# Performance work log

Measured on AMD Instinct MI355X. Metric: run time of the kernel, lower is better.

Reference implementation:

```python
import jax, jax.numpy as jnp
import numpy as np

# Lorentz (hyperboloid) manifold, curvature parameter K: x0 = sqrt(K + ||x_space||^2)
K = 1.0
LN_EPS = 1e-5
PROJ_EPS = 1e-6
L, D, H, B, S, V = 12, 512, 8, 2, 1024, 50257
DH = D // H  # 64 space dims per head


def add_time(space):
    # lift space components onto the hyperboloid
    t = jnp.sqrt(jnp.sum(space * space, axis=-1, keepdims=True) + K)
    return jnp.concatenate([t, space], axis=-1)


def l_project(z):
    # renormalize an ambient vector onto the hyperboloid (Lorentz midpoint / LResNet normalization)
    inner = -jnp.square(z[..., :1]) + jnp.sum(jnp.square(z[..., 1:]), axis=-1, keepdims=True)
    return jnp.sqrt(K) * z / jnp.sqrt(jnp.clip(-inner, PROJ_EPS, None))


def l_layernorm(x, g, b):
    # LayerNorm on the space part, recompute time
    s = x[..., 1:]
    mu = jnp.mean(s, axis=-1, keepdims=True)
    var = jnp.var(s, axis=-1, keepdims=True)
    s = (s - mu) * jax.lax.rsqrt(var + LN_EPS) * g + b
    return add_time(s)


def setup_inputs() -> dict:
    key = jax.random.key(0)
    ks = jax.random.split(key, 12)
    std_in = D ** -0.5
    std_out = (2 * D * L) ** -0.5  # out_proj_std from the torch init
    inp = {}
    inp['text_tokens'] = jax.random.randint(ks[0], (B, S), 0, V)
    inp['embed_table'] = jax.random.normal(ks[1], (V, D - 1), jnp.float32) * 0.02
    inp['Wq'] = jax.random.normal(ks[2], (L, D, D), jnp.float32) * std_in
    inp['bq'] = jnp.zeros((L, D), jnp.float32)
    inp['Wk'] = jax.random.normal(ks[3], (L, D, D), jnp.float32) * std_in
    inp['bk'] = jnp.zeros((L, D), jnp.float32)
    inp['Wv'] = jax.random.normal(ks[4], (L, D, D), jnp.float32) * std_in
    inp['bv'] = jnp.zeros((L, D), jnp.float32)
    inp['Wo'] = jax.random.normal(ks[5], (L, H * (DH + 1), D - 1), jnp.float32) * std_in
    inp['bo'] = jnp.zeros((L, D - 1), jnp.float32)
    inp['ln1_g'] = jnp.ones((L, D - 1), jnp.float32)
    inp['ln1_b'] = jnp.zeros((L, D - 1), jnp.float32)
    inp['ln2_g'] = jnp.ones((L, D - 1), jnp.float32)
    inp['ln2_b'] = jnp.zeros((L, D - 1), jnp.float32)
    inp['Wfc'] = jax.random.normal(ks[6], (L, D, 4 * D - 1), jnp.float32) * std_in
    inp['bfc'] = jnp.zeros((L, 4 * D - 1), jnp.float32)
    inp['Wpr'] = jax.random.normal(ks[7], (L, 4 * D, D - 1), jnp.float32) * std_out
    inp['bpr'] = jnp.zeros((L, D - 1), jnp.float32)
    inp['res_w1'] = jnp.ones((L,), jnp.float32)
    inp['res_w2'] = jnp.ones((L,), jnp.float32)
    inp['Wfin'] = jax.random.normal(ks[8], (D, D - 1), jnp.float32) * std_in
    inp['bfin'] = jnp.zeros((D - 1,), jnp.float32)
    inp['lnf_g'] = jnp.ones((D - 1,), jnp.float32)
    inp['lnf_b'] = jnp.zeros((D - 1,), jnp.float32)
    return inp


def reference(text_tokens, embed_table, Wq, bq, Wk, bk, Wv, bv, Wo, bo, ln1_g, ln1_b,
              ln2_g, ln2_b, Wfc, bfc, Wpr, bpr, res_w1, res_w2, Wfin, bfin, lnf_g, lnf_b):
    b, s = text_tokens.shape
    scale = 1.0 / np.sqrt(DH)
    # LorentzEmbeddings: space-part lookup, time recomputed
    x = add_time(embed_table[text_tokens])  # [B, S, D]
    causal = jnp.tril(jnp.ones((s, s), bool))  # True = attend
    for i in range(L):
        # --- Lorentz multi-head self-attention ---
        lx = l_layernorm(x, ln1_g[i], ln1_b[i])
        q = add_time((lx @ Wq[i] + bq[i]).reshape(b, s, H, DH))  # [B,S,H,DH+1]
        k = add_time((lx @ Wk[i] + bk[i]).reshape(b, s, H, DH))
        v = add_time((lx @ Wv[i] + bv[i]).reshape(b, s, H, DH))
        qm = jnp.concatenate([-q[..., :1], q[..., 1:]], axis=-1)  # apply Minkowski metric
        linner = jnp.einsum('bihd,bjhd->bhij', qm, k)  # Lorentz inner product <q_i, k_j>_L
        scores = (2.0 * K + 2.0 * linner) * scale     # = -d_L^2(q,k)/sqrt(dh)
        scores = jnp.where(causal[None, None], scores, -1e9)
        a = jax.nn.softmax(scores, axis=-1)
        agg = jnp.einsum('bhij,bjhd->bihd', a, v)      # Lorentz centroid numerator
        agg = l_project(agg)                           # normalize back to hyperboloid
        ax = add_time(agg.reshape(b, s, H * (DH + 1)) @ Wo[i] + bo[i])  # heads-concat proj
        x = l_project(x + res_w1[i] * ax)              # LResNet residual 1
        # --- Lorentz MLP ---
        h = l_layernorm(x, ln2_g[i], ln2_b[i])
        h = add_time(h @ Wfc[i] + bfc[i])              # c_fc: D -> 4D ambient
        h = add_time(jax.nn.gelu(h[..., 1:]))          # LorentzActivation (GELU on space)
        h = add_time(h @ Wpr[i] + bpr[i])              # c_proj: 4D -> D ambient
        x = l_project(x + res_w2[i] * h)               # LResNet residual 2
    x = add_time(x @ Wfin + bfin)                      # final_proj
    x = l_layernorm(x, lnf_g, lnf_b)                   # ln_final
    return x
```

## Files before the change

kernel.cpp:

```cpp
#include <hip/hip_runtime.h>
#include <cstdint>

#define DEV __device__ __forceinline__

typedef _Float16 f16;
typedef _Float16 f16x8 __attribute__((ext_vector_type(8)));
typedef float f32x4 __attribute__((ext_vector_type(4)));
typedef unsigned int u32;

DEV void gll16(const void* g, void* l) {
  __builtin_amdgcn_global_load_lds((const __attribute__((address_space(1))) u32*)g,
                                   (__attribute__((address_space(3))) u32*)l, 16, 0, 0);
}

DEV float block_sum(float v, float* red) {
#pragma unroll
  for (int o = 32; o; o >>= 1) v += __shfl_xor(v, o);
  int w = threadIdx.x >> 6;
  __syncthreads();
  if ((threadIdx.x & 63) == 0) red[w] = v;
  __syncthreads();
  return red[0] + red[1] + red[2] + red[3];
}

__global__ void k_trans(const float* __restrict__ W0, f16* __restrict__ BT0, int K, int N, int Kpad,
                        size_t srcStride, size_t dstStride) {
  __shared__ float t[32][33];
  const float* W = W0 + (size_t)blockIdx.z * srcStride;
  f16* BT = BT0 + (size_t)blockIdx.z * dstStride;
  int n0 = blockIdx.x * 32, k0 = blockIdx.y * 32, tx = threadIdx.x, ty = threadIdx.y;
  for (int i = ty; i < 32; i += 8) {
    int k = k0 + i, n = n0 + tx;
    t[i][tx] = (k < K && n < N) ? W[(size_t)k * N + n] : 0.f;
  }
  __syncthreads();
  for (int i = ty; i < 32; i += 8)
    BT[(size_t)(n0 + i) * Kpad + k0 + tx] = (f16)t[tx][i];
}

__global__ void k_trans3(const float* __restrict__ Wq, const float* __restrict__ Wk,
                         const float* __restrict__ Wv, f16* __restrict__ BT) {
  __shared__ float t[32][33];
  const int layer = blockIdx.z / 3, typ = blockIdx.z % 3;
  const float* W = ((typ == 0) ? Wq : (typ == 1) ? Wk : Wv) + (size_t)layer * 262144;
  f16* dst = BT + (size_t)layer * 786432 + (size_t)typ * 262144;
  int n0 = blockIdx.x * 32, k0 = blockIdx.y * 32, tx = threadIdx.x, ty = threadIdx.y;
  for (int i = ty; i < 32; i += 8) t[i][tx] = W[(size_t)(k0 + i) * 512 + n0 + tx];
  __syncthreads();
  for (int i = ty; i < 32; i += 8) dst[(size_t)(n0 + i) * 512 + k0 + tx] = (f16)t[tx][i];
}

template <int BM, int BN, int EPI>
__launch_bounds__(256)
__global__ void k_gemm(const f16* __restrict__ A, const f16* __restrict__ BT,
                       int lda, int ldb, int klen,
                       float* __restrict__ O1, float* __restrict__ O2, int ldc,
                       const float* __restrict__ c0, const float* __restrict__ c1,
                       const float* __restrict__ c2, float* __restrict__ ssq,
                       f16* __restrict__ H1, f16* __restrict__ H2, f16* __restrict__ H3) {
  constexpr int FM = BM / 32, FN = BN / 32;
  __shared__ f16 sA[BM * 64];
  __shared__ f16 sB[BN * 64];
  const int tid = threadIdx.x, wid = tid >> 6, lane = tid & 63;
  const int l15 = lane & 15, l4 = lane >> 4;
  const int m0 = blockIdx.x * BM, n0 = blockIdx.y * BN;
  const int wm = wid >> 1, wn = wid & 1;
  const int kbeg = blockIdx.z * klen;
  f32x4 acc[FM][FN];
#pragma unroll
  for (int i = 0; i < FM; i++)
#pragma unroll
    for (int j = 0; j < FN; j++) acc[i][j] = (f32x4){0.f, 0.f, 0.f, 0.f};
  const size_t ldab = (size_t)lda * 2, ldbb = (size_t)ldb * 2;
  const int swz = ((lane & 7) ^ (lane >> 3)) * 16;
  const char* Ab = (const char*)A + (size_t)m0 * ldab + (size_t)(lane >> 3) * ldab + swz;
  const char* Bb = (const char*)BT + (size_t)n0 * ldbb + (size_t)(lane >> 3) * ldbb + swz;
  for (int k0 = kbeg; k0 < kbeg + klen; k0 += 64) {
    for (int i = wid; i < BM / 8; i += 4)
      gll16(Ab + (size_t)(i * 8) * ldab + (size_t)k0 * 2, (char*)sA + i * 1024);
    for (int i = wid; i < BN / 8; i += 4)
      gll16(Bb + (size_t)(i * 8) * ldbb + (size_t)k0 * 2, (char*)sB + i * 1024);
    __syncthreads();
#pragma unroll
    for (int kk = 0; kk < 2; kk++) {
      f16x8 af[FM], bf[FN];
#pragma unroll
      for (int i = 0; i < FM; i++) {
        int row = wm * (BM / 2) + i * 16 + l15;
        af[i] = *(const f16x8*)(sA + row * 64 + (((kk * 4 + l4) ^ (l15 & 7)) * 8));
      }
#pragma unroll
      for (int j = 0; j < FN; j++) {
        int row = wn * (BN / 2) + j * 16 + l15;
        bf[j] = *(const f16x8*)(sB + row * 64 + (((kk * 4 + l4) ^ (l15 & 7)) * 8));
      }
#pragma unroll
      for (int i = 0; i < FM; i++)
#pragma unroll
        for (int j = 0; j < FN; j++)
          acc[i][j] = __builtin_amdgcn_mfma_f32_16x16x32_f16(af[i], bf[j], acc[i][j], 0, 0, 0);
    }
    __syncthreads();
  }
  if (EPI == 0) {
#pragma unroll
    for (int i = 0; i < FM; i++) {
      int row0 = m0 + wm * (BM / 2) + i * 16 + l4 * 4;
#pragma unroll
      for (int j = 0; j < FN; j++) {
        int col = n0 + wn * (BN / 2) + j * 16 + l15;
#pragma unroll
        for (int r = 0; r < 4; r++) O1[(size_t)(row0 + r) * ldc + col] = acc[i][j][r];
      }
    }
  } else if (EPI == 1) {
    const int cb = (n0 >> 6) + wn;
    const int typ = cb >> 3, h = cb & 7;
    const float* bb = (typ == 0) ? c0 : (typ == 1) ? c1 : c2;
    float bias_j[FN];
#pragma unroll
    for (int j = 0; j < FN; j++) bias_j[j] = bb[h * 64 + j * 16 + l15];
    const float qs = (typ == 0) ? 0.25f : 1.0f;
#pragma unroll
    for (int i = 0; i < FM; i++) {
#pragma unroll
      for (int r = 0; r < 4; r++) {
        float y[FN];
        float ss = 0.f;
#pragma unroll
        for (int j = 0; j < FN; j++) {
          y[j] = acc[i][j][r] + bias_j[j];
          ss += y[j] * y[j];
        }
        ss += __shfl_xor(ss, 1); ss += __shfl_xor(ss, 2);
        ss += __shfl_xor(ss, 4); ss += __shfl_xor(ss, 8);
        float t = sqrtf(ss + 1.f);
        int row = m0 + wm * 64 + i * 16 + l4 * 4 + r;
        int b = row >> 10, s = row & 1023, bh = b * 8 + h;
        if (typ < 2) {
          f16* dst = (typ == 0) ? H1 : H2;
          size_t base = ((size_t)bh * 1024 + s) * 88;
#pragma unroll
          for (int j = 0; j < FN; j++) dst[base + j * 16 + l15] = (f16)(qs * y[j]);
          if (l15 == 0) dst[base + 64] = (f16)(qs * t);
        } else {
#pragma unroll
          for (int j = 0; j < FN; j++)
            H3[((size_t)bh * 80 + j * 16 + l15) * 1024 + s] = (f16)y[j];
          if (l15 == 0) H3[((size_t)bh * 80 + 64) * 1024 + s] = (f16)t;
        }
      }
    }
  } else if (EPI == 2) {
#pragma unroll
    for (int i = 0; i < FM; i++) {
#pragma unroll
      for (int r = 0; r < 4; r++) {
        int row = m0 + wm * 64 + i * 16 + l4 * 4 + r;
        float ss = 0.f;
#pragma unroll
        for (int j = 0; j < FN; j++) {
          int col = n0 + wn * 64 + j * 16 + l15;
          float gg = 0.f;
          if (col < 2047) {
            float yv = acc[i][j][r] + c0[col];
            float cc = yv * yv * yv;
            gg = 0.5f * yv * (1.f + tanhf(0.7978845608f * (yv + 0.044715f * cc)));
          }
          ss += gg * gg;
          H1[(size_t)row * 2048 + col] = (f16)gg;
        }
        ss += __shfl_xor(ss, 1); ss += __shfl_xor(ss, 2);
        ss += __shfl_xor(ss, 4); ss += __shfl_xor(ss, 8);
        if (l15 == 0) atomicAdd(ssq + row, ss);
      }
    }
  } else {
    float* O = blockIdx.z ? O2 : O1;
#pragma unroll
    for (int i = 0; i < FM; i++) {
#pragma unroll
      for (int r = 0; r < 4; r++) {
        int row = m0 + wm * (BM / 2) + i * 16 + l4 * 4 + r;
        float t = 0.f;
        if (blockIdx.z == 0) t = sqrtf(ssq[row] + 1.f);
#pragma unroll
        for (int j = 0; j < FN; j++) {
          int col = n0 + wn * (BN / 2) + j * 16 + l15;
          float v = acc[i][j][r];
          if (blockIdx.z == 0) v += t * ((col < 511) ? c0[col] : 0.f);
          O[(size_t)row * ldc + col] = v;
        }
      }
    }
  }
}

__global__ void k_embed(const int* __restrict__ tok, const float* __restrict__ tbl,
                        const float* __restrict__ g, const float* __restrict__ bsh,
                        float* __restrict__ x, f16* __restrict__ act) {
  __shared__ float red[4];
  const int m = blockIdx.x, tid = threadIdx.x;
  const float* e = tbl + (size_t)tok[m] * 511;
  float e0 = (tid < 511) ? e[tid] : 0.f;
  float e1 = (tid + 256 < 511) ? e[tid + 256] : 0.f;
  float s1 = block_sum(e0 + e1, red);
  float s2 = block_sum(e0 * e0 + e1 * e1, red);
  float t = sqrtf(s2 + 1.f);
  float* xr = x + (size_t)m * 512;
  if (tid == 0) xr[0] = t;
  if (tid < 511) xr[1 + tid] = e0;
  if (tid + 256 < 511) xr[257 + tid] = e1;
  float mu = s1 / 511.f;
  float var = s2 / 511.f - mu * mu;
  float inv = rsqrtf(var + 1e-5f);
  float n0 = (tid < 511) ? (e0 - mu) * inv * g[tid] + bsh[tid] : 0.f;
  float n1 = (tid + 256 < 511) ? (e1 - mu) * inv * g[tid + 256] + bsh[tid + 256] : 0.f;
  float sn = block_sum(n0 * n0 + n1 * n1, red);
  float t2 = sqrtf(sn + 1.f);
  f16* ar = act + (size_t)m * 512;
  if (tid == 0) ar[0] = (f16)t2;
  if (tid < 511) ar[1 + tid] = (f16)n0;
  if (tid + 256 < 511) ar[257 + tid] = (f16)n1;
}

__launch_bounds__(64)
__global__ void k_attn(const f16* __restrict__ qhat, const f16* __restrict__ khat,
                       const f16* __restrict__ vT, f16* __restrict__ ao) {
  __shared__ f16 sP[16 * 88];
  const int bid = blockIdx.x, bh = bid & 15, rt = 63 - (bid >> 4);
  const int lane = threadIdx.x, l15 = lane & 15, l4 = lane >> 4;
  const f16* qp = qhat + ((size_t)bh * 1024 + rt * 16) * 88;
  const f16* kp = khat + (size_t)bh * 1024 * 88;
  const f16* vp = vT + (size_t)bh * 80 * 1024;
  f16x8 qf0 = *(const f16x8*)(qp + l15 * 88 + l4 * 8);
  f16x8 qf1 = *(const f16x8*)(qp + l15 * 88 + 32 + l4 * 8);
  float qth[4];
#pragma unroll
  for (int r = 0; r < 4; r++) qth[r] = (float)qp[(l4 * 4 + r) * 88 + 64];
  f32x4 acc[5];
#pragma unroll
  for (int i = 0; i < 5; i++) acc[i] = (f32x4){0, 0, 0, 0};
  float mrun[4] = {-3e38f, -3e38f, -3e38f, -3e38f}, lrun[4] = {0, 0, 0, 0};
  const int nt = (rt >> 2) + 1;
  for (int jt = 0; jt < nt; ++jt) {
    const int j0 = jt * 64;
    const bool dt = (jt == nt - 1);
    f32x4 sc[4];
#pragma unroll
    for (int fn = 0; fn < 4; fn++) {
      const f16* kb = kp + (size_t)(j0 + fn * 16 + l15) * 88;
      f16x8 k0v = *(const f16x8*)(kb + l4 * 8);
      f16x8 k1v = *(const f16x8*)(kb + 32 + l4 * 8);
      f32x4 a = (f32x4){0, 0, 0, 0};
      a = __builtin_amdgcn_mfma_f32_16x16x32_f16(qf0, k0v, a, 0, 0, 0);
      a = __builtin_amdgcn_mfma_f32_16x16x32_f16(qf1, k1v, a, 0, 0, 0);
      sc[fn] = a;
    }
    float s[4][4];
#pragma unroll
    for (int fn = 0; fn < 4; fn++) {
      float ktc = (float)kp[(size_t)(j0 + fn * 16 + l15) * 88 + 64];
      int col = j0 + fn * 16 + l15;
#pragma unroll
      for (int r = 0; r < 4; r++) {
        int row = rt * 16 + l4 * 4 + r;
        float v = sc[fn][r] - qth[r] * ktc;
        s[fn][r] = (!dt || col <= row) ? v : -3e38f;
      }
    }
    float mnew[4], al[4], rs[4];
#pragma unroll
    for (int r = 0; r < 4; r++) {
      float t = fmaxf(fmaxf(s[0][r], s[1][r]), fmaxf(s[2][r], s[3][r]));
#pragma unroll
      for (int o = 8; o; o >>= 1) t = fmaxf(t, __shfl_xor(t, o));
      mnew[r] = fmaxf(mrun[r], t);
      al[r] = exp2f((mrun[r] - mnew[r]) * 1.44269504f);
      mrun[r] = mnew[r];
      rs[r] = 0.f;
    }
#pragma unroll
    for (int fn = 0; fn < 4; fn++)
#pragma unroll
      for (int r = 0; r < 4; r++) {
        float p = exp2f((s[fn][r] - mnew[r]) * 1.44269504f);
        rs[r] += p;
        sP[(l4 * 4 + r) * 88 + fn * 16 + l15] = (f16)p;
      }
#pragma unroll
    for (int r = 0; r < 4; r++) {
#pragma unroll
      for (int o = 8; o; o >>= 1) rs[r] += __shfl_xor(rs[r], o);
      lrun[r] = lrun[r] * al[r] + rs[r];
    }
#pragma unroll
    for (int fd = 0; fd < 5; fd++)
#pragma unroll
      for (int r = 0; r < 4; r++) acc[fd][r] *= al[r];
    __syncthreads();
#pragma unroll
    for (int ks = 0; ks < 2; ks++) {
      f16x8 pf = *(const f16x8*)(sP + l15 * 88 + ks * 32 + l4 * 8);
#pragma unroll
      for (int fd = 0; fd < 5; fd++) {
        f16x8 vf = *(const f16x8*)(vp + (size_t)(fd * 16 + l15) * 1024 + j0 + ks * 32 + l4 * 8);
        acc[fd] = __builtin_amdgcn_mfma_f32_16x16x32_f16(pf, vf, acc[fd], 0, 0, 0);
      }
    }
    __syncthreads();
  }
  const int b = bh >> 3, h = bh & 7;
#pragma unroll
  for (int r = 0; r < 4; r++) {
    float invl = 1.0f / lrun[r];
    float ss = 0.f;
    float ov[4];
#pragma unroll
    for (int fd = 0; fd < 4; fd++) {
      ov[fd] = acc[fd][r] * invl;
      ss += ov[fd] * ov[fd];
    }
#pragma unroll
    for (int o = 8; o; o >>= 1) ss += __shfl_xor(ss, o);
    float tv = acc[4][r] * invl;
    tv = __shfl(tv, lane & 48);
    float scp = rsqrtf(fmaxf(tv * tv - ss, 1e-6f));
    int row = rt * 16 + l4 * 4 + r;
    size_t rowbase = ((size_t)b * 1024 + row) * 576;
    size_t rb = rowbase + h * 65;
    if (l15 == 0) ao[rb] = (f16)(tv * scp);
#pragma unroll
    for (int fd = 0; fd < 4; fd++) ao[rb + 1 + fd * 16 + l15] = (f16)(ov[fd] * scp);
    for (int c = l15; c < 56; c += 16) ao[rowbase + 520 + c] = (f16)0.f;
  }
}

__global__ void k_resproj(float* __restrict__ x, const float* __restrict__ r1,
                          const float* __restrict__ r2, int useR2,
                          const float* __restrict__ bias, const float* __restrict__ resw, int li,
                          const float* __restrict__ g, const float* __restrict__ bsh,
                          f16* __restrict__ act, int applyLN, float* __restrict__ ssq) {
  __shared__ float red[4];
  const int m = blockIdx.x, tid = threadIdx.x;
  const float* ra = r1 + (size_t)m * 512;
  const float* rb = r2 + (size_t)m * 512;
  float* xr = x + (size_t)m * 512;
  const float rw = resw[li];
  if (tid == 0) ssq[m] = 0.f;
  float y0 = 0.f, y1 = 0.f;
  if (tid < 511) { y0 = ra[tid] + bias[tid]; if (useR2) y0 += rb[tid]; }
  if (tid + 256 < 511) { y1 = ra[tid + 256] + bias[tid + 256]; if (useR2) y1 += rb[tid + 256]; }
  float s2 = block_sum(y0 * y0 + y1 * y1, red);
  float tax = sqrtf(s2 + 1.f);
  float xt = xr[0];
  float u0 = (tid < 511) ? xr[1 + tid] + rw * y0 : 0.f;
  float u1 = (tid + 256 < 511) ? xr[257 + tid] + rw * y1 : 0.f;
  float ut = xt + rw * tax;
  float su = block_sum(u0 + u1, red);
  float su2 = block_sum(u0 * u0 + u1 * u1, red);
  float scp = rsqrtf(fmaxf(ut * ut - su2, 1e-6f));
  float nx0 = u0 * scp, nx1 = u1 * scp, nxt = ut * scp;
  if (tid == 0) xr[0] = nxt;
  if (tid < 511) xr[1 + tid] = nx0;
  if (tid + 256 < 511) xr[257 + tid] = nx1;
  f16* ar = act + (size_t)m * 512;
  if (applyLN) {
    float mu = su * scp / 511.f;
    float var = su2 * scp * scp / 511.f - mu * mu;
    float inv = rsqrtf(var + 1e-5f);
    float n0 = (tid < 511) ? (nx0 - mu) * inv * g[tid] + bsh[tid] : 0.f;
    float n1 = (tid + 256 < 511) ? (nx1 - mu) * inv * g[tid + 256] + bsh[tid + 256] : 0.f;
    float sn = block_sum(n0 * n0 + n1 * n1, red);
    float t2 = sqrtf(sn + 1.f);
    if (tid == 0) ar[0] = (f16)t2;
    if (tid < 511) ar[1 + tid] = (f16)n0;
    if (tid + 256 < 511) ar[257 + tid] = (f16)n1;
  } else {
    if (tid == 0) ar[0] = (f16)nxt;
    if (tid < 511) ar[1 + tid] = (f16)nx0;
    if (tid + 256 < 511) ar[257 + tid] = (f16)nx1;
  }
}

__global__ void k_final(const float* __restrict__ raw, const float* __restrict__ bias,
                        const float* __restrict__ g, const float* __restrict__ bsh,
                        float* __restrict__ out) {
  __shared__ float red[4];
  const int m = blockIdx.x, tid = threadIdx.x;
  const float* rr = raw + (size_t)m * 512;
  float y0 = (tid < 511) ? rr[tid] + bias[tid] : 0.f;
  float y1 = (tid + 256 < 511) ? rr[tid + 256] + bias[tid + 256] : 0.f;
  float s1 = block_sum(y0 + y1, red);
  float s2 = block_sum(y0 * y0 + y1 * y1, red);
  float mu = s1 / 511.f;
  float var = s2 / 511.f - mu * mu;
  float inv = rsqrtf(var + 1e-5f);
  float n0 = (tid < 511) ? (y0 - mu) * inv * g[tid] + bsh[tid] : 0.f;
  float n1 = (tid + 256 < 511) ? (y1 - mu) * inv * g[tid + 256] + bsh[tid + 256] : 0.f;
  float sn = block_sum(n0 * n0 + n1 * n1, red);
  float t2 = sqrtf(sn + 1.f);
  float* orow = out + (size_t)m * 512;
  if (tid == 0) orow[0] = t2;
  if (tid < 511) orow[1 + tid] = n0;
  if (tid + 256 < 511) orow[257 + tid] = n1;
}

extern "C" void kernel_launch(void* const* d_in, const int* in_sizes, int n_in,
                              void* d_out, int out_size, void* d_ws, size_t ws_size,
                              hipStream_t stream) {
  (void)in_sizes; (void)n_in; (void)out_size; (void)ws_size;
  const int* tok = (const int*)d_in[0];
  const float* etab = (const float*)d_in[1];
  const float* Wq = (const float*)d_in[2];
  const float* bq = (const float*)d_in[3];
  const float* Wk = (const float*)d_in[4];
  const float* bk = (const float*)d_in[5];
  const float* Wv = (const float*)d_in[6];
  const float* bv = (const float*)d_in[7];
  const float* Wo = (const float*)d_in[8];
  const float* bo = (const float*)d_in[9];
  const float* ln1g = (const float*)d_in[10];
  const float* ln1b = (const float*)d_in[11];
  const float* ln2g = (const float*)d_in[12];
  const float* ln2b = (const float*)d_in[13];
  const float* Wfc = (const float*)d_in[14];
  const float* bfc = (const float*)d_in[15];
  const float* Wpr = (const float*)d_in[16];
  const float* bpr = (const float*)d_in[17];
  const float* rw1 = (const float*)d_in[18];
  const float* rw2 = (const float*)d_in[19];
  const float* Wfin = (const float*)d_in[20];
  const float* bfin = (const float*)d_in[21];
  const float* lnfg = (const float*)d_in[22];
  const float* lnfb = (const float*)d_in[23];

  char* wsb = (char*)d_ws;
  size_t off = 0;
  auto alloc = [&](size_t bytes) -> char* {
    char* p = wsb + off;
    off = (off + bytes + 1023) & ~(size_t)1023;
    return p;
  };
  float* x = (float*)alloc(2048ull * 512 * 4);
  f16* actA = (f16*)alloc(2048ull * 512 * 2);
  float* raw1 = (float*)alloc(2048ull * 512 * 4);
  float* raw2 = (float*)alloc(2048ull * 512 * 4);
  float* ssq = (float*)alloc(2048ull * 4);
  f16* qhat = (f16*)alloc(16ull * 1024 * 88 * 2);
  f16* khat = (f16*)alloc(16ull * 1024 * 88 * 2);
  f16* vT = (f16*)alloc(16ull * 80 * 1024 * 2);
  f16* ao = (f16*)alloc(2048ull * 576 * 2);
  f16* fcact = (f16*)alloc(2048ull * 2048 * 2);
  f16* wqkvT = (f16*)alloc(12ull * 1536 * 512 * 2);
  f16* woT = (f16*)alloc(12ull * 512 * 576 * 2);
  f16* wfcT = (f16*)alloc(12ull * 2048 * 512 * 2);
  f16* wprT = (f16*)alloc(12ull * 512 * 2048 * 2);
  f16* wfinT = (f16*)alloc(512ull * 512 * 2);

  k_trans3<<<dim3(16, 16, 36), dim3(32, 8), 0, stream>>>(Wq, Wk, Wv, wqkvT);
  k_trans<<<dim3(16, 18, 12), dim3(32, 8), 0, stream>>>(Wo, woT, 520, 511, 576,
                                                        520ull * 511, 512ull * 576);
  k_trans<<<dim3(64, 16, 12), dim3(32, 8), 0, stream>>>(Wfc, wfcT, 512, 2047, 512,
                                                        512ull * 2047, 2048ull * 512);
  k_trans<<<dim3(16, 64, 12), dim3(32, 8), 0, stream>>>(Wpr + 511, wprT, 2047, 511, 2048,
                                                        2048ull * 511, 512ull * 2048);
  k_trans<<<dim3(16, 16, 1), dim3(32, 8), 0, stream>>>(Wfin, wfinT, 512, 511, 512, 0, 0);

  k_embed<<<2048, 256, 0, stream>>>(tok, etab, ln1g, ln1b, x, actA);

  for (int li = 0; li < 12; li++) {
    const f16* wqkvT_l = wqkvT + (size_t)li * 1536 * 512;
    const f16* woT_l = woT + (size_t)li * 512 * 576;
    const f16* wfcT_l = wfcT + (size_t)li * 2048 * 512;
    const f16* wprT_l = wprT + (size_t)li * 512 * 2048;
    const float* Wpr_l = Wpr + (size_t)li * 2048 * 511;
    const float* bq_l = bq + (size_t)li * 512;
    const float* bk_l = bk + (size_t)li * 512;
    const float* bv_l = bv + (size_t)li * 512;
    const float* bo_l = bo + (size_t)li * 511;
    const float* bfc_l = bfc + (size_t)li * 2047;
    const float* bpr_l = bpr + (size_t)li * 511;
    const float* ln2g_l = ln2g + (size_t)li * 511;
    const float* ln2b_l = ln2b + (size_t)li * 511;

    k_gemm<128, 128, 1><<<dim3(16, 12, 1), 256, 0, stream>>>(
        actA, wqkvT_l, 512, 512, 512, nullptr, nullptr, 0,
        bq_l, bk_l, bv_l, nullptr, qhat, khat, vT);
    k_attn<<<1024, 64, 0, stream>>>(qhat, khat, vT, ao);
    k_gemm<64, 64, 0><<<dim3(32, 8, 1), 256, 0, stream>>>(
        ao, woT_l, 576, 576, 576, raw1, nullptr, 512,
        nullptr, nullptr, nullptr, nullptr, nullptr, nullptr, nullptr);
    k_resproj<<<2048, 256, 0, stream>>>(x, raw1, raw1, 0, bo_l, rw1, li,
                                        ln2g_l, ln2b_l, actA, 1, ssq);
    k_gemm<128, 128, 2><<<dim3(16, 16, 1), 256, 0, stream>>>(
        actA, wfcT_l, 512, 512, 512, nullptr, nullptr, 0,
        bfc_l, nullptr, nullptr, ssq, fcact, nullptr, nullptr);
    k_gemm<64, 64, 3><<<dim3(32, 8, 2), 256, 0, stream>>>(
        fcact, wprT_l, 2048, 2048, 1024, raw1, raw2, 512,
        Wpr_l, nullptr, nullptr, ssq, nullptr, nullptr, nullptr);
    const float* ng = (li < 11) ? ln1g + (size_t)(li + 1) * 511 : ln1g;
    const float* nb = (li < 11) ? ln1b + (size_t)(li + 1) * 511 : ln1b;
    k_resproj<<<2048, 256, 0, stream>>>(x, raw1, raw2, 1, bpr_l, rw2, li,
                                        ng, nb, actA, (li < 11) ? 1 : 0, ssq);
  }

  k_gemm<64, 64, 0><<<dim3(32, 8, 1), 256, 0, stream>>>(
      actA, wfinT, 512, 512, 512, raw1, nullptr, 512,
      nullptr, nullptr, nullptr, nullptr, nullptr, nullptr, nullptr);
  k_final<<<2048, 256, 0, stream>>>(raw1, bfin, lnfg, lnfb, (float*)d_out);
}
```

Measured before the change: 1.650 ms.

## Fuse whole forward pass into a persistent megakernel with grid barriers

```diff
diff --git a/kernel.cpp b/kernel.cpp
--- a/kernel.cpp
+++ b/kernel.cpp
@@ -1,151 +1,183 @@
 #include <hip/hip_runtime.h>
 #include <cstdint>
-
-#define DEV __device__ __forceinline__
 
 typedef _Float16 f16;
 typedef _Float16 f16x8 __attribute__((ext_vector_type(8)));
 typedef float f32x4 __attribute__((ext_vector_type(4)));
 typedef unsigned int u32;
 
+#define DEV __device__ __forceinline__
+
 DEV void gll16(const void* g, void* l) {
   __builtin_amdgcn_global_load_lds((const __attribute__((address_space(1))) u32*)g,
                                    (__attribute__((address_space(3))) u32*)l, 16, 0, 0);
 }
 
-DEV float block_sum(float v, float* red) {
+DEV float wsum(float v) {
 #pragma unroll
   for (int o = 32; o; o >>= 1) v += __shfl_xor(v, o);
-  int w = threadIdx.x >> 6;
+  return v;
+}
+
+struct MP {
+  const int* tok; const float* etab;
+  const float* Wq; const float* bq; const float* Wk; const float* bk;
+  const float* Wv; const float* bv; const float* Wo; const float* bo;
+  const float* ln1g; const float* ln1b; const float* ln2g; const float* ln2b;
+  const float* Wfc; const float* bfc; const float* Wpr; const float* bpr;
+  const float* rw1; const float* rw2; const float* Wfin; const float* bfin;
+  const float* lnfg; const float* lnfb;
+  f16* actA; float* rawA; float* rawB; float* rawC; float* rawD; float* ssq;
+  f16* qhat; f16* khat; f16* vT; f16* ao; f16* fcact;
+  f16* wqkvT; f16* woT; f16* wfcT; f16* wprT; f16* wfinT;
+  u32* bar; float* out;
+};
+
+DEV void gbar(const MP& p) {
   __syncthreads();
-  if ((threadIdx.x & 63) == 0) red[w] = v;
+  if (threadIdx.x == 0) {
+    u32* c8 = p.bar + (blockIdx.x & 7) * 32;
+    u32* root = p.bar + 256;
+    u32* gen = p.bar + 260;
+    u32 g = __hip_atomic_load(gen, __ATOMIC_RELAXED, __HIP_MEMORY_SCOPE_AGENT);
+    __threadfence();
+    u32 a = __hip_atomic_fetch_add(c8, 1u, __ATOMIC_ACQ_REL, __HIP_MEMORY_SCOPE_AGENT);
+    if (a == 31u) {
+      __hip_atomic_store(c8, 0u, __ATOMIC_RELAXED, __HIP_MEMORY_SCOPE_AGENT);
+      u32 b = __hip_atomic_fetch_add(root, 1u, __ATOMIC_ACQ_REL, __HIP_MEMORY_SCOPE_AGENT);
+      if (b == 7u) {
+        __hip_atomic_store(root, 0u, __ATOMIC_RELAXED, __HIP_MEMORY_SCOPE_AGENT);
+        __hip_atomic_store(gen, g + 1u, __ATOMIC_RELEASE, __HIP_MEMORY_SCOPE_AGENT);
+      } else {
+        for (int it = 0; it < (1 << 22); ++it) {
+          if (__hip_atomic_load(gen, __ATOMIC_ACQUIRE, __HIP_MEMORY_SCOPE_AGENT) != g) break;
+          __builtin_amdgcn_s_sleep(4);
+        }
+      }
+    } else {
+      for (int it = 0; it < (1 << 22); ++it) {
+        if (__hip_atomic_load(gen, __ATOMIC_ACQUIRE, __HIP_MEMORY_SCOPE_AGENT) != g) break;
+        __builtin_amdgcn_s_sleep(4);
+      }
+    }
+    __threadfence();
+  }
   __syncthreads();
-  return red[0] + red[1] + red[2] + red[3];
-}
-
-__global__ void k_trans(const float* __restrict__ W0, f16* __restrict__ BT0, int K, int N, int Kpad,
-                        size_t srcStride, size_t dstStride) {
-  __shared__ float t[32][33];
-  const float* W = W0 + (size_t)blockIdx.z * srcStride;
-  f16* BT = BT0 + (size_t)blockIdx.z * dstStride;
-  int n0 = blockIdx.x * 32, k0 = blockIdx.y * 32, tx = threadIdx.x, ty = threadIdx.y;
-  for (int i = ty; i < 32; i += 8) {
-    int k = k0 + i, n = n0 + tx;
-    t[i][tx] = (k < K && n < N) ? W[(size_t)k * N + n] : 0.f;
+}
+
+DEV void trans_tile(const float* W, f16* BT, int K, int N, int ldk, int n0, int k0,
+                    char* SM) {
+  float* tile = (float*)SM;
+  const int tid = threadIdx.x;
+  const int c = tid & 63, r0 = tid >> 6;
+#pragma unroll
+  for (int i = 0; i < 8; i++) {
+    int kr = r0 + i * 8;
+    int k = k0 + kr, n = n0 + c;
+    tile[kr * 65 + c] = (k < K && n < N) ? W[(size_t)k * N + n] : 0.f;
   }
   __syncthreads();
-  for (int i = ty; i < 32; i += 8)
-    BT[(size_t)(n0 + i) * Kpad + k0 + tx] = (f16)t[tx][i];
-}
-
-__global__ void k_trans3(const float* __restrict__ Wq, const float* __restrict__ Wk,
-                         const float* __restrict__ Wv, f16* __restrict__ BT) {
-  __shared__ float t[32][33];
-  const int layer = blockIdx.z / 3, typ = blockIdx.z % 3;
-  const float* W = ((typ == 0) ? Wq : (typ == 1) ? Wk : Wv) + (size_t)layer * 262144;
-  f16* dst = BT + (size_t)layer * 786432 + (size_t)typ * 262144;
-  int n0 = blockIdx.x * 32, k0 = blockIdx.y * 32, tx = threadIdx.x, ty = threadIdx.y;
-  for (int i = ty; i < 32; i += 8) t[i][tx] = W[(size_t)(k0 + i) * 512 + n0 + tx];
+#pragma unroll
+  for (int i = 0; i < 8; i++) {
+    int nn = r0 + i * 8;
+    BT[(size_t)(n0 + nn) * ldk + k0 + c] = (f16)tile[c * 65 + nn];
+  }
   __syncthreads();
-  for (int i = ty; i < 32; i += 8) dst[(size_t)(n0 + i) * 512 + k0 + tx] = (f16)t[tx][i];
-}
-
-template <int BM, int BN, int EPI>
-__launch_bounds__(256)
-__global__ void k_gemm(const f16* __restrict__ A, const f16* __restrict__ BT,
-                       int lda, int ldb, int klen,
-                       float* __restrict__ O1, float* __restrict__ O2, int ldc,
-                       const float* __restrict__ c0, const float* __restrict__ c1,
-                       const float* __restrict__ c2, float* __restrict__ ssq,
-                       f16* __restrict__ H1, f16* __restrict__ H2, f16* __restrict__ H3) {
-  constexpr int FM = BM / 32, FN = BN / 32;
-  __shared__ f16 sA[BM * 64];
-  __shared__ f16 sB[BN * 64];
+}
+
+template <int EPI>
+DEV void gemm_task(const f16* A, const f16* B, int lda, int ldb, int tm, int tn,
+                   int kbeg, int ksteps, float* O, const float* c0, const float* c1,
+                   const float* c2, float* ssq, f16* H1, f16* H2, f16* H3,
+                   int addR1, char* SM) {
   const int tid = threadIdx.x, wid = tid >> 6, lane = tid & 63;
   const int l15 = lane & 15, l4 = lane >> 4;
-  const int m0 = blockIdx.x * BM, n0 = blockIdx.y * BN;
-  const int wm = wid >> 1, wn = wid & 1;
-  const int kbeg = blockIdx.z * klen;
-  f32x4 acc[FM][FN];
-#pragma unroll
-  for (int i = 0; i < FM; i++)
-#pragma unroll
-    for (int j = 0; j < FN; j++) acc[i][j] = (f32x4){0.f, 0.f, 0.f, 0.f};
+  const int wm = wid & 3, wn = wid >> 2;
+  const int m0 = tm * 128, n0 = tn * 128;
+  f32x4 acc[2][4];
+#pragma unroll
+  for (int i = 0; i < 2; i++)
+#pragma unroll
+    for (int j = 0; j < 4; j++) acc[i][j] = (f32x4){0.f, 0.f, 0.f, 0.f};
   const size_t ldab = (size_t)lda * 2, ldbb = (size_t)ldb * 2;
   const int swz = ((lane & 7) ^ (lane >> 3)) * 16;
-  const char* Ab = (const char*)A + (size_t)m0 * ldab + (size_t)(lane >> 3) * ldab + swz;
-  const char* Bb = (const char*)BT + (size_t)n0 * ldbb + (size_t)(lane >> 3) * ldbb + swz;
-  for (int k0 = kbeg; k0 < kbeg + klen; k0 += 64) {
-    for (int i = wid; i < BM / 8; i += 4)
-      gll16(Ab + (size_t)(i * 8) * ldab + (size_t)k0 * 2, (char*)sA + i * 1024);
-    for (int i = wid; i < BN / 8; i += 4)
-      gll16(Bb + (size_t)(i * 8) * ldbb + (size_t)k0 * 2, (char*)sB + i * 1024);
+  const char* Ab = (const char*)A + (size_t)(m0 + (lane >> 3)) * ldab + swz + (size_t)kbeg * 2;
+  const char* Bb = (const char*)B + (size_t)(n0 + (lane >> 3)) * ldbb + swz + (size_t)kbeg * 2;
+  auto stage = [&](int buf, int ks) {
+    char* da = SM + buf * 32768;
+    char* db = da + 16384;
+    for (int i = wid; i < 16; i += 8) gll16(Ab + (size_t)(i * 8) * ldab + ks * 128, da + i * 1024);
+    for (int i = wid; i < 16; i += 8) gll16(Bb + (size_t)(i * 8) * ldbb + ks * 128, db + i * 1024);
+  };
+  stage(0, 0);
+  __syncthreads();
+  int cur = 0;
+  for (int ks = 0; ks < ksteps; ks++) {
+    if (ks + 1 < ksteps) stage(cur ^ 1, ks + 1);
+    const f16* sA = (const f16*)(SM + cur * 32768);
+    const f16* sB = (const f16*)(SM + cur * 32768 + 16384);
+#pragma unroll
+    for (int kk = 0; kk < 2; kk++) {
+      f16x8 af[2], bf[4];
+#pragma unroll
+      for (int i = 0; i < 2; i++) {
+        int row = wm * 32 + i * 16 + l15;
+        af[i] = *(const f16x8*)(sA + row * 64 + (((kk * 4 + l4) ^ (l15 & 7)) * 8));
+      }
+#pragma unroll
+      for (int j = 0; j < 4; j++) {
+        int row = wn * 64 + j * 16 + l15;
+        bf[j] = *(const f16x8*)(sB + row * 64 + (((kk * 4 + l4) ^ (l15 & 7)) * 8));
+      }
+#pragma unroll
+      for (int i = 0; i < 2; i++)
+#pragma unroll
+        for (int j = 0; j < 4; j++)
+          acc[i][j] = __builtin_amdgcn_mfma_f32_16x16x32_f16(af[i], bf[j], acc[i][j], 0, 0, 0);
+    }
     __syncthreads();
-#pragma unroll
-    for (int kk = 0; kk < 2; kk++) {
-      f16x8 af[FM], bf[FN];
-#pragma unroll
-      for (int i = 0; i < FM; i++) {
-        int row = wm * (BM / 2) + i * 16 + l15;
-        af[i] = *(const f16x8*)(sA + row * 64 + (((kk * 4 + l4) ^ (l15 & 7)) * 8));
-      }
-#pragma unroll
-      for (int j = 0; j < FN; j++) {
-        int row = wn * (BN / 2) + j * 16 + l15;
-        bf[j] = *(const f16x8*)(sB + row * 64 + (((kk * 4 + l4) ^ (l15 & 7)) * 8));
-      }
-#pragma unroll
-      for (int i = 0; i < FM; i++)
-#pragma unroll
-        for (int j = 0; j < FN; j++)
-          acc[i][j] = __builtin_amdgcn_mfma_f32_16x16x32_f16(af[i], bf[j], acc[i][j], 0, 0, 0);
-    }
-    __syncthreads();
+    cur ^= 1;
   }
   if (EPI == 0) {
 #pragma unroll
-    for (int i = 0; i < FM; i++) {
-      int row0 = m0 + wm * (BM / 2) + i * 16 + l4 * 4;
-#pragma unroll
-      for (int j = 0; j < FN; j++) {
-        int col = n0 + wn * (BN / 2) + j * 16 + l15;
-#pragma unroll
-        for (int r = 0; r < 4; r++) O1[(size_t)(row0 + r) * ldc + col] = acc[i][j][r];
+    for (int i = 0; i < 2; i++) {
+      int row = m0 + wm * 32 + i * 16 + l4 * 4;
+#pragma unroll
+      for (int j = 0; j < 4; j++) {
+        int col = n0 + wn * 64 + j * 16 + l15;
+#pragma unroll
+        for (int r = 0; r < 4; r++) O[(size_t)(row + r) * 520 + col + 1] = acc[i][j][r];
       }
     }
   } else if (EPI == 1) {
     const int cb = (n0 >> 6) + wn;
     const int typ = cb >> 3, h = cb & 7;
     const float* bb = (typ == 0) ? c0 : (typ == 1) ? c1 : c2;
-    float bias_j[FN];
-#pragma unroll
-    for (int j = 0; j < FN; j++) bias_j[j] = bb[h * 64 + j * 16 + l15];
+    float bj[4];
+#pragma unroll
+    for (int j = 0; j < 4; j++) bj[j] = bb[h * 64 + j * 16 + l15];
     const float qs = (typ == 0) ? 0.25f : 1.0f;
 #pragma unroll
-    for (int i = 0; i < FM; i++) {
+    for (int i = 0; i < 2; i++) {
 #pragma unroll
       for (int r = 0; r < 4; r++) {
-        float y[FN];
-        float ss = 0.f;
-#pragma unroll
-        for (int j = 0; j < FN; j++) {
-          y[j] = acc[i][j][r] + bias_j[j];
-          ss += y[j] * y[j];
-        }
+        float y[4], ss = 0.f;
+#pragma unroll
+        for (int j = 0; j < 4; j++) { y[j] = acc[i][j][r] + bj[j]; ss += y[j] * y[j]; }
         ss += __shfl_xor(ss, 1); ss += __shfl_xor(ss, 2);
         ss += __shfl_xor(ss, 4); ss += __shfl_xor(ss, 8);
         float t = sqrtf(ss + 1.f);
-        int row = m0 + wm * 64 + i * 16 + l4 * 4 + r;
+        int row = m0 + wm * 32 + i * 16 + l4 * 4 + r;
         int b = row >> 10, s = row & 1023, bh = b * 8 + h;
         if (typ < 2) {
-          f16* dst = (typ == 0) ? H1 : H2;
+          f16* dst = typ ? H2 : H1;
           size_t base = ((size_t)bh * 1024 + s) * 88;
 #pragma unroll
-          for (int j = 0; j < FN; j++) dst[base + j * 16 + l15] = (f16)(qs * y[j]);
+          for (int j = 0; j < 4; j++) dst[base + j * 16 + l15] = (f16)(qs * y[j]);
           if (l15 == 0) dst[base + 64] = (f16)(qs * t);
         } else {
 #pragma unroll
-          for (int j = 0; j < FN; j++)
+          for (int j = 0; j < 4; j++)
             H3[((size_t)bh * 80 + j * 16 + l15) * 1024 + s] = (f16)y[j];
           if (l15 == 0) H3[((size_t)bh * 80 + 64) * 1024 + s] = (f16)t;
         }
@@ -153,19 +185,20 @@
     }
   } else if (EPI == 2) {
 #pragma unroll
-    for (int i = 0; i < FM; i++) {
+    for (int i = 0; i < 2; i++) {
 #pragma unroll
       for (int r = 0; r < 4; r++) {
-        int row = m0 + wm * 64 + i * 16 + l4 * 4 + r;
+        int row = m0 + wm * 32 + i * 16 + l4 * 4 + r;
         float ss = 0.f;
 #pragma unroll
-        for (int j = 0; j < FN; j++) {
+        for (int j = 0; j < 4; j++) {
           int col = n0 + wn * 64 + j * 16 + l15;
           float gg = 0.f;
           if (col < 2047) {
             float yv = acc[i][j][r] + c0[col];
-            float cc = yv * yv * yv;
-            gg = 0.5f * yv * (1.f + tanhf(0.7978845608f * (yv + 0.044715f * cc)));
+            float z = 0.7978845608f * (yv + 0.044715f * yv * yv * yv);
+            float th = 1.f - 2.f / (__expf(2.f * z) + 1.f);
+            gg = 0.5f * yv * (1.f + th);
           }
           ss += gg * gg;
           H1[(size_t)row * 2048 + col] = (f16)gg;
@@ -176,60 +209,30 @@
       }
     }
   } else {
-    float* O = blockIdx.z ? O2 : O1;
-#pragma unroll
-    for (int i = 0; i < FM; i++) {
+#pragma unroll
+    for (int i = 0; i < 2; i++) {
 #pragma unroll
       for (int r = 0; r < 4; r++) {
-        int row = m0 + wm * (BM / 2) + i * 16 + l4 * 4 + r;
-        float t = 0.f;
-        if (blockIdx.z == 0) t = sqrtf(ssq[row] + 1.f);
-#pragma unroll
-        for (int j = 0; j < FN; j++) {
-          int col = n0 + wn * (BN / 2) + j * 16 + l15;
+        int row = m0 + wm * 32 + i * 16 + l4 * 4 + r;
+        float t = addR1 ? sqrtf(ssq[row] + 1.f) : 0.f;
+#pragma unroll
+        for (int j = 0; j < 4; j++) {
+          int col = n0 + wn * 64 + j * 16 + l15;
           float v = acc[i][j][r];
-          if (blockIdx.z == 0) v += t * ((col < 511) ? c0[col] : 0.f);
-          O[(size_t)row * ldc + col] = v;
+          if (addR1) v += t * ((col < 511) ? c0[col] : 0.f);
+          O[(size_t)row * 520 + col + 1] = v;
         }
       }
     }
   }
 }
 
-__global__ void k_embed(const int* __restrict__ tok, const float* __restrict__ tbl,
-                        const float* __restrict__ g, const float* __restrict__ bsh,
-                        float* __restrict__ x, f16* __restrict__ act) {
-  __shared__ float red[4];
-  const int m = blockIdx.x, tid = threadIdx.x;
-  const float* e = tbl + (size_t)tok[m] * 511;
-  float e0 = (tid < 511) ? e[tid] : 0.f;
-  float e1 = (tid + 256 < 511) ? e[tid + 256] : 0.f;
-  float s1 = block_sum(e0 + e1, red);
-  float s2 = block_sum(e0 * e0 + e1 * e1, red);
-  float t = sqrtf(s2 + 1.f);
-  float* xr = x + (size_t)m * 512;
-  if (tid == 0) xr[0] = t;
-  if (tid < 511) xr[1 + tid] = e0;
-  if (tid + 256 < 511) xr[257 + tid] = e1;
-  float mu = s1 / 511.f;
-  float var = s2 / 511.f - mu * mu;
-  float inv = rsqrtf(var + 1e-5f);
-  float n0 = (tid < 511) ? (e0 - mu) * inv * g[tid] + bsh[tid] : 0.f;
-  float n1 = (tid + 256 < 511) ? (e1 - mu) * inv * g[tid + 256] + bsh[tid + 256] : 0.f;
-  float sn = block_sum(n0 * n0 + n1 * n1, red);
-  float t2 = sqrtf(sn + 1.f);
-  f16* ar = act + (size_t)m * 512;
-  if (tid == 0) ar[0] = (f16)t2;
-  if (tid < 511) ar[1 + tid] = (f16)n0;
-  if (tid + 256 < 511) ar[257 + tid] = (f16)n1;
-}
-
-__launch_bounds__(64)
-__global__ void k_attn(const f16* __restrict__ qhat, const f16* __restrict__ khat,
-                       const f16* __restrict__ vT, f16* __restrict__ ao) {
-  __shared__ f16 sP[16 * 88];
-  const int bid = blockIdx.x, bh = bid & 15, rt = 63 - (bid >> 4);
-  const int lane = threadIdx.x, l15 = lane & 15, l4 = lane >> 4;
+DEV void attn_task(int t, const f16* qhat, const f16* khat, const f16* vT, f16* ao,
+                   char* sPb) {
+  const int lane = threadIdx.x & 63;
+  const int bh = t & 15, rt = 63 - (t >> 4);
+  const int l15 = lane & 15, l4 = lane >> 4;
+  f16* sP = (f16*)sPb;
   const f16* qp = qhat + ((size_t)bh * 1024 + rt * 16) * 88;
   const f16* kp = khat + (size_t)bh * 1024 * 88;
   const f16* vp = vT + (size_t)bh * 80 * 1024;
@@ -272,10 +275,10 @@
     float mnew[4], al[4], rs[4];
 #pragma unroll
     for (int r = 0; r < 4; r++) {
-      float t = fmaxf(fmaxf(s[0][r], s[1][r]), fmaxf(s[2][r], s[3][r]));
-#pragma unroll
-      for (int o = 8; o; o >>= 1) t = fmaxf(t, __shfl_xor(t, o));
-      mnew[r] = fmaxf(mrun[r], t);
+      float tm = fmaxf(fmaxf(s[0][r], s[1][r]), fmaxf(s[2][r], s[3][r]));
+#pragma unroll
+      for (int o = 8; o; o >>= 1) tm = fmaxf(tm, __shfl_xor(tm, o));
+      mnew[r] = fmaxf(mrun[r], tm);
       al[r] = exp2f((mrun[r] - mnew[r]) * 1.44269504f);
       mrun[r] = mnew[r];
       rs[r] = 0.f;
@@ -284,9 +287,9 @@
     for (int fn = 0; fn < 4; fn++)
 #pragma unroll
       for (int r = 0; r < 4; r++) {
-        float p = exp2f((s[fn][r] - mnew[r]) * 1.44269504f);
-        rs[r] += p;
-        sP[(l4 * 4 + r) * 88 + fn * 16 + l15] = (f16)p;
+        float pv = exp2f((s[fn][r] - mnew[r]) * 1.44269504f);
+        rs[r] += pv;
+        sP[(l4 * 4 + r) * 88 + fn * 16 + l15] = (f16)pv;
       }
 #pragma unroll
     for (int r = 0; r < 4; r++) {
@@ -298,7 +301,8 @@
     for (int fd = 0; fd < 5; fd++)
 #pragma unroll
       for (int r = 0; r < 4; r++) acc[fd][r] *= al[r];
-    __syncthreads();
+    asm volatile("s_waitcnt lgkmcnt(0)" ::: "memory");
+    __builtin_amdgcn_sched_barrier(0);
 #pragma unroll
     for (int ks = 0; ks < 2; ks++) {
       f16x8 pf = *(const f16x8*)(sP + l15 * 88 + ks * 32 + l4 * 8);
@@ -308,205 +312,304 @@
         acc[fd] = __builtin_amdgcn_mfma_f32_16x16x32_f16(pf, vf, acc[fd], 0, 0, 0);
       }
     }
-    __syncthreads();
   }
   const int b = bh >> 3, h = bh & 7;
 #pragma unroll
   for (int r = 0; r < 4; r++) {
     float invl = 1.0f / lrun[r];
-    float ss = 0.f;
-    float ov[4];
-#pragma unroll
-    for (int fd = 0; fd < 4; fd++) {
-      ov[fd] = acc[fd][r] * invl;
-      ss += ov[fd] * ov[fd];
-    }
+    float ss = 0.f, ov[4];
+#pragma unroll
+    for (int fd = 0; fd < 4; fd++) { ov[fd] = acc[fd][r] * invl; ss += ov[fd] * ov[fd]; }
 #pragma unroll
     for (int o = 8; o; o >>= 1) ss += __shfl_xor(ss, o);
     float tv = acc[4][r] * invl;
     tv = __shfl(tv, lane & 48);
     float scp = rsqrtf(fmaxf(tv * tv - ss, 1e-6f));
     int row = rt * 16 + l4 * 4 + r;
-    size_t rowbase = ((size_t)b * 1024 + row) * 576;
-    size_t rb = rowbase + h * 65;
+    size_t rb = ((size_t)b * 1024 + row) * 640 + h * 65;
     if (l15 == 0) ao[rb] = (f16)(tv * scp);
 #pragma unroll
     for (int fd = 0; fd < 4; fd++) ao[rb + 1 + fd * 16 + l15] = (f16)(ov[fd] * scp);
-    for (int c = l15; c < 56; c += 16) ao[rowbase + 520 + c] = (f16)0.f;
-  }
-}
-
-__global__ void k_resproj(float* __restrict__ x, const float* __restrict__ r1,
-                          const float* __restrict__ r2, int useR2,
-                          const float* __restrict__ bias, const float* __restrict__ resw, int li,
-                          const float* __restrict__ g, const float* __restrict__ bsh,
-                          f16* __restrict__ act, int applyLN, float* __restrict__ ssq) {
-  __shared__ float red[4];
-  const int m = blockIdx.x, tid = threadIdx.x;
-  const float* ra = r1 + (size_t)m * 512;
-  const float* rb = r2 + (size_t)m * 512;
-  float* xr = x + (size_t)m * 512;
-  const float rw = resw[li];
-  if (tid == 0) ssq[m] = 0.f;
-  float y0 = 0.f, y1 = 0.f;
-  if (tid < 511) { y0 = ra[tid] + bias[tid]; if (useR2) y0 += rb[tid]; }
-  if (tid + 256 < 511) { y1 = ra[tid + 256] + bias[tid + 256]; if (useR2) y1 += rb[tid + 256]; }
-  float s2 = block_sum(y0 * y0 + y1 * y1, red);
-  float tax = sqrtf(s2 + 1.f);
-  float xt = xr[0];
-  float u0 = (tid < 511) ? xr[1 + tid] + rw * y0 : 0.f;
-  float u1 = (tid + 256 < 511) ? xr[257 + tid] + rw * y1 : 0.f;
-  float ut = xt + rw * tax;
-  float su = block_sum(u0 + u1, red);
-  float su2 = block_sum(u0 * u0 + u1 * u1, red);
+  }
+}
+
+DEV void resproj_row(float (&xreg)[8], int row, const float* rA, const float* rB,
+                     const float* rC, const float* rD, int np, const float* bias,
+                     float rw, const float* g, const float* bsh, f16* act, int applyLN,
+                     float* ssq) {
+  const int lane = threadIdx.x & 63, cbase = lane * 8;
+  const size_t rb = (size_t)row * 520 + cbase;
+  float y[8];
+  {
+    f32x4 a0 = *(const f32x4*)(rA + rb), a1 = *(const f32x4*)(rA + rb + 4);
+    f32x4 b0 = *(const f32x4*)(rB + rb), b1 = *(const f32x4*)(rB + rb + 4);
+#pragma unroll
+    for (int j = 0; j < 4; j++) { y[j] = a0[j] + b0[j]; y[4 + j] = a1[j] + b1[j]; }
+    if (np == 4) {
+      f32x4 c0v = *(const f32x4*)(rC + rb), c1v = *(const f32x4*)(rC + rb + 4);
+      f32x4 d0 = *(const f32x4*)(rD + rb), d1 = *(const f32x4*)(rD + rb + 4);
+#pragma unroll
+      for (int j = 0; j < 4; j++) { y[j] += c0v[j] + d0[j]; y[4 + j] += c1v[j] + d1[j]; }
+    }
+  }
+#pragma unroll
+  for (int j = 0; j < 8; j++) {
+    int c = cbase + j;
+    y[j] = (c >= 1) ? (y[j] + bias[c - 1]) : 0.f;
+  }
+  float lss = 0.f;
+#pragma unroll
+  for (int j = 0; j < 8; j++) lss += y[j] * y[j];
+  float tax = sqrtf(wsum(lss) + 1.f);
+  float u[8];
+#pragma unroll
+  for (int j = 0; j < 8; j++) u[j] = xreg[j] + rw * y[j];
+  if (lane == 0) u[0] = xreg[0] + rw * tax;
+  float lsu = 0.f, lsu2 = 0.f;
+#pragma unroll
+  for (int j = 0; j < 8; j++) { lsu += u[j]; lsu2 += u[j] * u[j]; }
+  if (lane == 0) { lsu -= u[0]; lsu2 -= u[0] * u[0]; }
+  float su = wsum(lsu), su2 = wsum(lsu2);
+  float ut = __shfl(u[0], 0);
   float scp = rsqrtf(fmaxf(ut * ut - su2, 1e-6f));
-  float nx0 = u0 * scp, nx1 = u1 * scp, nxt = ut * scp;
-  if (tid == 0) xr[0] = nxt;
-  if (tid < 511) xr[1 + tid] = nx0;
-  if (tid + 256 < 511) xr[257 + tid] = nx1;
-  f16* ar = act + (size_t)m * 512;
+  float nx[8];
+#pragma unroll
+  for (int j = 0; j < 8; j++) { nx[j] = u[j] * scp; xreg[j] = nx[j]; }
+  if (lane == 0) ssq[row] = 0.f;
+  f16* ar = act + (size_t)row * 512;
+  f16x8 ov;
   if (applyLN) {
-    float mu = su * scp / 511.f;
-    float var = su2 * scp * scp / 511.f - mu * mu;
+    float mu = su * scp * (1.f / 511.f);
+    float var = su2 * scp * scp * (1.f / 511.f) - mu * mu;
     float inv = rsqrtf(var + 1e-5f);
-    float n0 = (tid < 511) ? (nx0 - mu) * inv * g[tid] + bsh[tid] : 0.f;
-    float n1 = (tid + 256 < 511) ? (nx1 - mu) * inv * g[tid + 256] + bsh[tid + 256] : 0.f;
-    float sn = block_sum(n0 * n0 + n1 * n1, red);
-    float t2 = sqrtf(sn + 1.f);
-    if (tid == 0) ar[0] = (f16)t2;
-    if (tid < 511) ar[1 + tid] = (f16)n0;
-    if (tid + 256 < 511) ar[257 + tid] = (f16)n1;
+    float n[8], lsn = 0.f;
+#pragma unroll
+    for (int j = 0; j < 8; j++) {
+      int c = cbase + j;
+      float nv = (c >= 1) ? ((nx[j] - mu) * inv * g[c - 1] + bsh[c - 1]) : 0.f;
+      n[j] = nv; lsn += nv * nv;
+    }
+    float t2 = sqrtf(wsum(lsn) + 1.f);
+    if (lane == 0) n[0] = t2;
+#pragma unroll
+    for (int j = 0; j < 8; j++) ov[j] = (f16)n[j];
   } else {
-    if (tid == 0) ar[0] = (f16)nxt;
-    if (tid < 511) ar[1 + tid] = (f16)nx0;
-    if (tid + 256 < 511) ar[257 + tid] = (f16)nx1;
-  }
-}
-
-__global__ void k_final(const float* __restrict__ raw, const float* __restrict__ bias,
-                        const float* __restrict__ g, const float* __restrict__ bsh,
-                        float* __restrict__ out) {
-  __shared__ float red[4];
-  const int m = blockIdx.x, tid = threadIdx.x;
-  const float* rr = raw + (size_t)m * 512;
-  float y0 = (tid < 511) ? rr[tid] + bias[tid] : 0.f;
-  float y1 = (tid + 256 < 511) ? rr[tid + 256] + bias[tid + 256] : 0.f;
-  float s1 = block_sum(y0 + y1, red);
-  float s2 = block_sum(y0 * y0 + y1 * y1, red);
-  float mu = s1 / 511.f;
-  float var = s2 / 511.f - mu * mu;
+#pragma unroll
+    for (int j = 0; j < 8; j++) ov[j] = (f16)nx[j];
+  }
+  *(f16x8*)(ar + cbase) = ov;
+}
+
+DEV void embed_row(float (&xreg)[8], int row, const int* tok, const float* tbl,
+                   const float* g, const float* bsh, f16* act, float* ssq) {
+  const int lane = threadIdx.x & 63, cbase = lane * 8;
+  const float* e = tbl + (size_t)tok[row] * 511;
+  float ev[8];
+#pragma unroll
+  for (int j = 0; j < 8; j++) {
+    int c = cbase + j;
+    ev[j] = (c >= 1) ? e[c - 1] : 0.f;
+  }
+  float lss = 0.f, lsu = 0.f;
+#pragma unroll
+  for (int j = 0; j < 8; j++) { lss += ev[j] * ev[j]; lsu += ev[j]; }
+  float ss = wsum(lss), su = wsum(lsu);
+  float t = sqrtf(ss + 1.f);
+#pragma unroll
+  for (int j = 0; j < 8; j++) xreg[j] = ev[j];
+  if (lane == 0) xreg[0] = t;
+  float mu = su * (1.f / 511.f);
+  float var = ss * (1.f / 511.f) - mu * mu;
   float inv = rsqrtf(var + 1e-5f);
-  float n0 = (tid < 511) ? (y0 - mu) * inv * g[tid] + bsh[tid] : 0.f;
-  float n1 = (tid + 256 < 511) ? (y1 - mu) * inv * g[tid + 256] + bsh[tid + 256] : 0.f;
-  float sn = block_sum(n0 * n0 + n1 * n1, red);
-  float t2 = sqrtf(sn + 1.f);
-  float* orow = out + (size_t)m * 512;
-  if (tid == 0) orow[0] = t2;
-  if (tid < 511) orow[1 + tid] = n0;
-  if (tid + 256 < 511) orow[257 + tid] = n1;
+  float n[8], lsn = 0.f;
+#pragma unroll
+  for (int j = 0; j < 8; j++) {
+    int c = cbase + j;
+    float nv = (c >= 1) ? ((ev[j] - mu) * inv * g[c - 1] + bsh[c - 1]) : 0.f;
+    n[j] = nv; lsn += nv * nv;
+  }
+  float t2 = sqrtf(wsum(lsn) + 1.f);
+  if (lane == 0) n[0] = t2;
+  f16x8 ov;
+#pragma unroll
+  for (int j = 0; j < 8; j++) ov[j] = (f16)n[j];
+  *(f16x8*)(act + (size_t)row * 512 + cbase) = ov;
+  if (lane == 0) ssq[row] = 0.f;
+}
+
+DEV void final_row(int row, const float* raw, const float* bias, const float* g,
+                   const float* bsh, float* out) {
+  const int lane = threadIdx.x & 63, cbase = lane * 8;
+  const size_t rb = (size_t)row * 520 + cbase;
+  f32x4 a0 = *(const f32x4*)(raw + rb), a1 = *(const f32x4*)(raw + rb + 4);
+  float y[8];
+#pragma unroll
+  for (int j = 0; j < 4; j++) { y[j] = a0[j]; y[4 + j] = a1[j]; }
+  float lss = 0.f, lsu = 0.f;
+#pragma unroll
+  for (int j = 0; j < 8; j++) {
+    int c = cbase + j;
+    y[j] = (c >= 1) ? (y[j] + bias[c - 1]) : 0.f;
+    lss += y[j] * y[j]; lsu += y[j];
+  }
+  float s2 = wsum(lss), su = wsum(lsu);
+  float mu = su * (1.f / 511.f);
+  float var = s2 * (1.f / 511.f) - mu * mu;
+  float inv = rsqrtf(var + 1e-5f);
+  float n[8], lsn = 0.f;
+#pragma unroll
+  for (int j = 0; j < 8; j++) {
+    int c = cbase + j;
+    float nv = (c >= 1) ? ((y[j] - mu) * inv * g[c - 1] + bsh[c - 1]) : 0.f;
+    n[j] = nv; lsn += nv * nv;
+  }
+  float t2 = sqrtf(wsum(lsn) + 1.f);
+  if (lane == 0) n[0] = t2;
+  float* orow = out + (size_t)row * 512 + cbase;
+  f32x4 o0, o1;
+#pragma unroll
+  for (int j = 0; j < 4; j++) { o0[j] = n[j]; o1[j] = n[4 + j]; }
+  *(f32x4*)orow = o0;
+  *(f32x4*)(orow + 4) = o1;
+}
+
+__global__ __launch_bounds__(512, 2) void k_mega(MP p) {
+  const int wg = blockIdx.x, tid = threadIdx.x, wid = tid >> 6;
+  __shared__ __align__(16) char SM[65536];
+  float xreg[8];
+  const int myrow = wg * 8 + wid;
+
+  for (int t = wg; t < 9472; t += 256) {
+    const float* W; f16* D; int K, N, ldk, n0, k0;
+    if (t < 2304) {
+      int mat = t >> 6, tile = t & 63;
+      int layer = mat / 3, typ = mat % 3;
+      W = (typ == 0 ? p.Wq : typ == 1 ? p.Wk : p.Wv) + (size_t)layer * 262144;
+      D = p.wqkvT + (size_t)layer * 786432 + (size_t)typ * 262144;
+      K = 512; N = 512; ldk = 512; n0 = (tile >> 3) * 64; k0 = (tile & 7) * 64;
+    } else if (t < 3264) {
+      int id = t - 2304; int l = id / 80, tile = id % 80;
+      W = p.Wo + (size_t)l * 265720; D = p.woT + (size_t)l * 327680;
+      K = 520; N = 511; ldk = 640; n0 = (tile / 10) * 64; k0 = (tile % 10) * 64;
+    } else if (t < 6336) {
+      int id = t - 3264; int l = id >> 8, tile = id & 255;
+      W = p.Wfc + (size_t)l * 1048064; D = p.wfcT + (size_t)l * 1048576;
+      K = 512; N = 2047; ldk = 512; n0 = (tile >> 3) * 64; k0 = (tile & 7) * 64;
+    } else if (t < 9408) {
+      int id = t - 6336; int l = id >> 8, tile = id & 255;
+      W = p.Wpr + (size_t)l * 1046528 + 511; D = p.wprT + (size_t)l * 1048576;
+      K = 2047; N = 511; ldk = 2048; n0 = (tile >> 5) * 64; k0 = (tile & 31) * 64;
+    } else {
+      int id = t - 9408;
+      W = p.Wfin; D = p.wfinT; K = 512; N = 511; ldk = 512;
+      n0 = (id >> 3) * 64; k0 = (id & 7) * 64;
+    }
+    trans_tile(W, D, K, N, ldk, n0, k0, SM);
+  }
+  for (int i = wg * 512 + tid; i < 2048 * 120; i += 256 * 512)
+    p.ao[(size_t)(i / 120) * 640 + 520 + (i % 120)] = (f16)0.f;
+  embed_row(xreg, myrow, p.tok, p.etab, p.ln1g, p.ln1b, p.actA, p.ssq);
+  gbar(p);
+
+  for (int li = 0; li < 12; li++) {
+    const f16* wqkvT_l = p.wqkvT + (size_t)li * 786432;
+    const f16* woT_l = p.woT + (size_t)li * 327680;
+    const f16* wfcT_l = p.wfcT + (size_t)li * 1048576;
+    const f16* wprT_l = p.wprT + (size_t)li * 1048576;
+    const float* bq_l = p.bq + li * 512;
+    const float* bk_l = p.bk + li * 512;
+    const float* bv_l = p.bv + li * 512;
+    const float* bo_l = p.bo + li * 511;
+    const float* bfc_l = p.bfc + li * 2047;
+    const float* bpr_l = p.bpr + li * 511;
+    const float* w0_l = p.Wpr + (size_t)li * 1046528;
+
+    for (int t = wg; t < 192; t += 256)
+      gemm_task<1>(p.actA, wqkvT_l, 512, 512, t / 12, t % 12, 0, 8, nullptr,
+                   bq_l, bk_l, bv_l, nullptr, p.qhat, p.khat, p.vT, 0, SM);
+    gbar(p);
+    if (wid < 4) attn_task(wid * 256 + wg, p.qhat, p.khat, p.vT, p.ao, SM + wid * 2816);
+    gbar(p);
+    for (int t = wg; t < 128; t += 256) {
+      int tm = t >> 3, tn = (t >> 1) & 3, tz = t & 1;
+      gemm_task<0>(p.ao, woT_l, 640, 640, tm, tn, tz * 320, 5,
+                   tz ? p.rawB : p.rawA, nullptr, nullptr, nullptr, nullptr,
+                   nullptr, nullptr, nullptr, 0, SM);
+    }
+    gbar(p);
+    resproj_row(xreg, myrow, p.rawA, p.rawB, nullptr, nullptr, 2, bo_l, p.rw1[li],
+                p.ln2g + li * 511, p.ln2b + li * 511, p.actA, 1, p.ssq);
+    gbar(p);
+    for (int t = wg; t < 256; t += 256)
+      gemm_task<2>(p.actA, wfcT_l, 512, 512, t >> 4, t & 15, 0, 8, nullptr,
+                   bfc_l, nullptr, nullptr, p.ssq, p.fcact, nullptr, nullptr, 0, SM);
+    gbar(p);
+    for (int t = wg; t < 256; t += 256) {
+      int tm = t >> 4, tn = (t >> 2) & 3, tz = t & 3;
+      float* O = tz == 0 ? p.rawA : tz == 1 ? p.rawB : tz == 2 ? p.rawC : p.rawD;
+      gemm_task<3>(p.fcact, wprT_l, 2048, 2048, tm, tn, tz * 512, 8, O,
+                   w0_l, nullptr, nullptr, p.ssq, nullptr, nullptr, nullptr, tz == 0, SM);
+    }
+    gbar(p);
+    const float* ng = (li < 11) ? p.ln1g + (li + 1) * 511 : p.ln1g;
+    const float* nb = (li < 11) ? p.ln1b + (li + 1) * 511 : p.ln1b;
+    resproj_row(xreg, myrow, p.rawA, p.rawB, p.rawC, p.rawD, 4, bpr_l, p.rw2[li],
+                ng, nb, p.actA, (li < 11) ? 1 : 0, p.ssq);
+    gbar(p);
+  }
+
+  for (int t = wg; t < 64; t += 256)
+    gemm_task<0>(p.actA, p.wfinT, 512, 512, t >> 2, t & 3, 0, 8, p.rawA,
+                 nullptr, nullptr, nullptr, nullptr, nullptr, nullptr, nullptr, 0, SM);
+  gbar(p);
+  final_row(myrow, p.rawA, p.bfin, p.lnfg, p.lnfb, p.out);
 }
 
 extern "C" void kernel_launch(void* const* d_in, const int* in_sizes, int n_in,
                               void* d_out, int out_size, void* d_ws, size_t ws_size,
                               hipStream_t stream) {
   (void)in_sizes; (void)n_in; (void)out_size; (void)ws_size;
-  const int* tok = (const int*)d_in[0];
-  const float* etab = (const float*)d_in[1];
-  const float* Wq = (const float*)d_in[2];
-  const float* bq = (const float*)d_in[3];
-  const float* Wk = (const float*)d_in[4];
-  const float* bk = (const float*)d_in[5];
-  const float* Wv = (const float*)d_in[6];
-  const float* bv = (const float*)d_in[7];
-  const float* Wo = (const float*)d_in[8];
-  const float* bo = (const float*)d_in[9];
-  const float* ln1g = (const float*)d_in[10];
-  const float* ln1b = (const float*)d_in[11];
-  const float* ln2g = (const float*)d_in[12];
-  const float* ln2b = (const float*)d_in[13];
-  const float* Wfc = (const float*)d_in[14];
-  const float* bfc = (const float*)d_in[15];
-  const float* Wpr = (const float*)d_in[16];
-  const float* bpr = (const float*)d_in[17];
-  const float* rw1 = (const float*)d_in[18];
-  const float* rw2 = (const float*)d_in[19];
-  const float* Wfin = (const float*)d_in[20];
-  const float* bfin = (const float*)d_in[21];
-  const float* lnfg = (const float*)d_in[22];
-  const float* lnfb = (const float*)d_in[23];
+  MP p;
+  p.tok = (const int*)d_in[0];
+  p.etab = (const float*)d_in[1];
+  p.Wq = (const float*)d_in[2];  p.bq = (const float*)d_in[3];
+  p.Wk = (const float*)d_in[4];  p.bk = (const float*)d_in[5];
+  p.Wv = (const float*)d_in[6];  p.bv = (const float*)d_in[7];
+  p.Wo = (const float*)d_in[8];  p.bo = (const float*)d_in[9];
+  p.ln1g = (const float*)d_in[10]; p.ln1b = (const float*)d_in[11];
+  p.ln2g = (const float*)d_in[12]; p.ln2b = (const float*)d_in[13];
+  p.Wfc = (const float*)d_in[14]; p.bfc = (const float*)d_in[15];
+  p.Wpr = (const float*)d_in[16]; p.bpr = (const float*)d_in[17];
+  p.rw1 = (const float*)d_in[18]; p.rw2 = (const float*)d_in[19];
+  p.Wfin = (const float*)d_in[20]; p.bfin = (const float*)d_in[21];
+  p.lnfg = (const float*)d_in[22]; p.lnfb = (const float*)d_in[23];
 
   char* wsb = (char*)d_ws;
   size_t off = 0;
   auto alloc = [&](size_t bytes) -> char* {
-    char* p = wsb + off;
+    char* q = wsb + off;
     off = (off + bytes + 1023) & ~(size_t)1023;
-    return p;
+    return q;
   };
-  float* x = (float*)alloc(2048ull * 512 * 4);
-  f16* actA = (f16*)alloc(2048ull * 512 * 2);
-  float* raw1 = (float*)alloc(2048ull * 512 * 4);
-  float* raw2 = (float*)alloc(2048ull * 512 * 4);
-  float* ssq = (float*)alloc(2048ull * 4);
-  f16* qhat = (f16*)alloc(16ull * 1024 * 88 * 2);
-  f16* khat = (f16*)alloc(16ull * 1024 * 88 * 2);
-  f16* vT = (f16*)alloc(16ull * 80 * 1024 * 2);
-  f16* ao = (f16*)alloc(2048ull * 576 * 2);
-  f16* fcact = (f16*)alloc(2048ull * 2048 * 2);
-  f16* wqkvT = (f16*)alloc(12ull * 1536 * 512 * 2);
-  f16* woT = (f16*)alloc(12ull * 512 * 576 * 2);
-  f16* wfcT = (f16*)alloc(12ull * 2048 * 512 * 2);
-  f16* wprT = (f16*)alloc(12ull * 512 * 2048 * 2);
-  f16* wfinT = (f16*)alloc(512ull * 512 * 2);
-
-  k_trans3<<<dim3(16, 16, 36), dim3(32, 8), 0, stream>>>(Wq, Wk, Wv, wqkvT);
-  k_trans<<<dim3(16, 18, 12), dim3(32, 8), 0, stream>>>(Wo, woT, 520, 511, 576,
-                                                        520ull * 511, 512ull * 576);
-  k_trans<<<dim3(64, 16, 12), dim3(32, 8), 0, stream>>>(Wfc, wfcT, 512, 2047, 512,
-                                                        512ull * 2047, 2048ull * 512);
-  k_trans<<<dim3(16, 64, 12), dim3(32, 8), 0, stream>>>(Wpr + 511, wprT, 2047, 511, 2048,
-                                                        2048ull * 511, 512ull * 2048);
-  k_trans<<<dim3(16, 16, 1), dim3(32, 8), 0, stream>>>(Wfin, wfinT, 512, 511, 512, 0, 0);
-
-  k_embed<<<2048, 256, 0, stream>>>(tok, etab, ln1g, ln1b, x, actA);
-
-  for (int li = 0; li < 12; li++) {
-    const f16* wqkvT_l = wqkvT + (size_t)li * 1536 * 512;
-    const f16* woT_l = woT + (size_t)li * 512 * 576;
-    const f16* wfcT_l = wfcT + (size_t)li * 2048 * 512;
-    const f16* wprT_l = wprT + (size_t)li * 512 * 2048;
-    const float* Wpr_l = Wpr + (size_t)li * 2048 * 511;
-    const float* bq_l = bq + (size_t)li * 512;
-    const float* bk_l = bk + (size_t)li * 512;
-    const float* bv_l = bv + (size_t)li * 512;
-    const float* bo_l = bo + (size_t)li * 511;
-    const float* bfc_l = bfc + (size_t)li * 2047;
-    const float* bpr_l = bpr + (size_t)li * 511;
-    const float* ln2g_l = ln2g + (size_t)li * 511;
-    const float* ln2b_l = ln2b + (size_t)li * 511;
-
-    k_gemm<128, 128, 1><<<dim3(16, 12, 1), 256, 0, stream>>>(
-        actA, wqkvT_l, 512, 512, 512, nullptr, nullptr, 0,
-        bq_l, bk_l, bv_l, nullptr, qhat, khat, vT);
-    k_attn<<<1024, 64, 0, stream>>>(qhat, khat, vT, ao);
-    k_gemm<64, 64, 0><<<dim3(32, 8, 1), 256, 0, stream>>>(
-        ao, woT_l, 576, 576, 576, raw1, nullptr, 512,
-        nullptr, nullptr, nullptr, nullptr, nullptr, nullptr, nullptr);
-    k_resproj<<<2048, 256, 0, stream>>>(x, raw1, raw1, 0, bo_l, rw1, li,
-                                        ln2g_l, ln2b_l, actA, 1, ssq);
-    k_gemm<128, 128, 2><<<dim3(16, 16, 1), 256, 0, stream>>>(
-        actA, wfcT_l, 512, 512, 512, nullptr, nullptr, 0,
-        bfc_l, nullptr, nullptr, ssq, fcact, nullptr, nullptr);
-    k_gemm<64, 64, 3><<<dim3(32, 8, 2), 256, 0, stream>>>(
-        fcact, wprT_l, 2048, 2048, 1024, raw1, raw2, 512,
-        Wpr_l, nullptr, nullptr, ssq, nullptr, nullptr, nullptr);
-    const float* ng = (li < 11) ? ln1g + (size_t)(li + 1) * 511 : ln1g;
-    const float* nb = (li < 11) ? ln1b + (size_t)(li + 1) * 511 : ln1b;
-    k_resproj<<<2048, 256, 0, stream>>>(x, raw1, raw2, 1, bpr_l, rw2, li,
-                                        ng, nb, actA, (li < 11) ? 1 : 0, ssq);
-  }
-
-  k_gemm<64, 64, 0><<<dim3(32, 8, 1), 256, 0, stream>>>(
-      actA, wfinT, 512, 512, 512, raw1, nullptr, 512,
-      nullptr, nullptr, nullptr, nullptr, nullptr, nullptr, nullptr);
-  k_final<<<2048, 256, 0, stream>>>(raw1, bfin, lnfg, lnfb, (float*)d_out);
-}
+  p.actA = (f16*)alloc(2048ull * 512 * 2);
+  p.rawA = (float*)alloc(2048ull * 520 * 4);
+  p.rawB = (float*)alloc(2048ull * 520 * 4);
+  p.rawC = (float*)alloc(2048ull * 520 * 4);
+  p.rawD = (float*)alloc(2048ull * 520 * 4);
+  p.ssq = (float*)alloc(2048ull * 4);
+  p.qhat = (f16*)alloc(16ull * 1024 * 88 * 2);
+  p.khat = (f16*)alloc(16ull * 1024 * 88 * 2);
+  p.vT = (f16*)alloc(16ull * 80 * 1024 * 2);
+  p.ao = (f16*)alloc(2048ull * 640 * 2);
+  p.fcact = (f16*)alloc(2048ull * 2048 * 2);
+  p.wqkvT = (f16*)alloc(12ull * 786432 * 2);
+  p.woT = (f16*)alloc(12ull * 327680 * 2);
+  p.wfcT = (f16*)alloc(12ull * 1048576 * 2);
+  p.wprT = (f16*)alloc(12ull * 1048576 * 2);
+  p.wfinT = (f16*)alloc(512ull * 512 * 2);
+  p.bar = (u32*)alloc(4096);
+  p.out = (float*)d_out;
+
+  hipMemsetAsync(p.bar, 0, 4096, stream);
+  k_mega<<<256, 512, 0, stream>>>(p);
+}
```

After: 5.428 ms. +228.9%, slower.
